# Optimization experiments

Measured on AMD Instinct MI355X. Metric: run time of the kernel, lower is better.

Reference implementation:

```python
import jax, jax.numpy as jnp
import numpy as np

EPS = 1e-12  # matches torch F.normalize default eps

def _l2_normalize(v, axis=-1):
    n = jnp.sqrt(jnp.sum(v * v, axis=axis, keepdims=True))
    return v / jnp.maximum(n, EPS)

def setup_inputs() -> dict:
    key = jax.random.key(0)
    k1, k2, k3 = jax.random.split(key, 3)
    B, S, D_IN, D_OUT, T = 4, 4096, 1024, 1024, 1024
    std = 1.0 / np.sqrt(D_IN)
    return {
        "x": jax.random.normal(k1, (B, S, D_IN), dtype=jnp.float32),
        "key_tokens": jax.random.normal(k2, (T, D_IN), dtype=jnp.float32) * std,
        "value_tokens": jax.random.normal(k3, (T, D_OUT), dtype=jnp.float32) * std,
        "temp": jnp.ones((T, 1), dtype=jnp.float32),
    }

def reference(x, key_tokens, value_tokens, temp):
    # x: [B,S,D_in]; key_tokens: [T,D_in]; value_tokens: [T,D_out]; temp: [T,1]
    x_norm = _l2_normalize(x)                      # [B,S,D_in]
    k_norm = _l2_normalize(key_tokens)             # [T,D_in]
    sim = jnp.einsum('bsd,td->bst', x_norm, k_norm)  # [B,S,T]
    sim = sim * jax.nn.sigmoid(temp).reshape(1, 1, -1)
    # mod_softmax: scale each row to RMS-norm sqrt(T), then exact GELU
    T = sim.shape[-1]
    scale = jnp.sqrt(jnp.float32(T)) / jnp.sqrt(jnp.sum(sim * sim, axis=-1, keepdims=True))
    weights = jax.nn.gelu(sim * scale, approximate=False)  # [B,S,T]
    return jnp.einsum('bst,to->bso', weights, value_tokens)  # [B,S,D_out]
```

## Files before the change

kernel.cpp:

```cpp
#include <hip/hip_runtime.h>
#include <math.h>

typedef __attribute__((ext_vector_type(8))) short short8;
typedef __attribute__((ext_vector_type(4))) float floatx4;

__device__ __forceinline__ float bf2f(unsigned short u) {
    union { unsigned int u; float f; } v;
    v.u = ((unsigned int)u) << 16;
    return v.f;
}

__device__ __forceinline__ unsigned short f2bf(float f) {
    union { float f; unsigned int u; } v;
    v.f = f;
    unsigned int r = v.u + 0x7fffu + ((v.u >> 16) & 1u);
    return (unsigned short)(r >> 16);
}

__device__ __forceinline__ void gload16_lds(const void* g, void* l) {
    __builtin_amdgcn_global_load_lds(
        (const __attribute__((address_space(1))) unsigned int*)g,
        (__attribute__((address_space(3))) unsigned int*)l, 16, 0, 0);
}

__device__ __forceinline__ ushort4 cvt4(float4 v, float fa) {
    ushort4 o;
    o.x = f2bf(v.x * fa); o.y = f2bf(v.y * fa);
    o.z = f2bf(v.z * fa); o.w = f2bf(v.w * fa);
    return o;
}

__global__ __launch_bounds__(256) void prep_kernel(
    const float* __restrict__ x, const float* __restrict__ key,
    const float* __restrict__ temp, const float* __restrict__ val,
    unsigned short* __restrict__ xb, unsigned short* __restrict__ kf,
    unsigned short* __restrict__ VT, float* __restrict__ rowsq,
    int M, int T, int D, int Dout, int nRowBlocks) {
    const int bid = blockIdx.x;
    if (bid < nRowBlocks) {
        const int lane = threadIdx.x & 63;
        const int nWaves = nRowBlocks << 2;
        const int totRows = M + T;
        for (int row = (bid << 2) | (int)(threadIdx.x >> 6); row < totRows;
             row += nWaves) {
            const bool isx = row < M;
            const int r = isx ? row : row - M;
            const float4* s4 =
                (const float4*)(isx ? (x + (size_t)r * D) : (key + (size_t)r * D));
            float4 v0 = s4[lane];
            float4 v1 = s4[lane + 64];
            float4 v2 = s4[lane + 128];
            float4 v3 = s4[lane + 192];
            float s = v0.x * v0.x + v0.y * v0.y + v0.z * v0.z + v0.w * v0.w;
            s += v1.x * v1.x + v1.y * v1.y + v1.z * v1.z + v1.w * v1.w;
            s += v2.x * v2.x + v2.y * v2.y + v2.z * v2.z + v2.w * v2.w;
            s += v3.x * v3.x + v3.y * v3.y + v3.z * v3.z + v3.w * v3.w;
#pragma unroll
            for (int o = 32; o > 0; o >>= 1) s += __shfl_xor(s, o, 64);
            float fa = 1.0f / fmaxf(sqrtf(s), 1e-12f);
            if (isx) {
                if (lane == 0) rowsq[r] = 0.0f;
            } else {
                fa = fa / (1.0f + expf(-temp[r]));
            }
            ushort4* dst =
                (ushort4*)(isx ? (xb + (size_t)r * D) : (kf + (size_t)r * D));
            dst[lane] = cvt4(v0, fa);
            dst[lane + 64] = cvt4(v1, fa);
            dst[lane + 128] = cvt4(v2, fa);
            dst[lane + 192] = cvt4(v3, fa);
        }
    } else {
        __shared__ unsigned short tile[64][65];
        const int idx = bid - nRowBlocks;
        const int nCt = Dout >> 6;
        const int c0 = (idx % nCt) * 64;
        const int r0 = (idx / nCt) * 64;
        const int t = threadIdx.x;
        for (int i = t; i < 4096; i += 256) {
            int rr = i >> 6, cc = i & 63;
            tile[rr][cc] = f2bf(val[(size_t)(r0 + rr) * Dout + c0 + cc]);
        }
        __syncthreads();
        for (int i = t; i < 4096; i += 256) {
            int rr = i >> 6, cc = i & 63;
            VT[(size_t)(c0 + rr) * T + r0 + cc] = tile[cc][rr];
        }
    }
}

template <int MODE>
__global__ __launch_bounds__(256) void gemm_bt(const unsigned short* __restrict__ A,
                                               const unsigned short* __restrict__ B,
                                               void* __restrict__ Cv,
                                               float* __restrict__ rowsq,
                                               int M, int N, int K) {
    __shared__ __align__(16) unsigned short As[128 * 64];
    __shared__ __align__(16) unsigned short Bs[128 * 64];
    const int tid = threadIdx.x;
    const int lane = tid & 63;
    const int w = tid >> 6;
    const int m0 = blockIdx.x * 128;
    const int n0 = blockIdx.y * 128;
    const int wm = (w & 1) * 64;
    const int wn = (w >> 1) * 64;
    const int cl = lane & 15;
    const int q = lane >> 4;

    floatx4 acc[4][4];
#pragma unroll
    for (int i = 0; i < 4; i++)
#pragma unroll
        for (int j = 0; j < 4; j++) acc[i][j] = (floatx4){0.f, 0.f, 0.f, 0.f};

    const int srow = tid >> 2;
    const int skof = (tid & 3) * 8;
    const unsigned short* ga0 = A + (size_t)(m0 + srow) * K + skof;
    const unsigned short* ga1 = A + (size_t)(m0 + srow + 64) * K + skof;
    const unsigned short* gb0 = B + (size_t)(n0 + srow) * K + skof;
    const unsigned short* gb1 = B + (size_t)(n0 + srow + 64) * K + skof;
    unsigned short* la0 = &As[(w * 64) * 8];
    unsigned short* la1 = &As[(256 + w * 64) * 8];
    unsigned short* lb0 = &Bs[(w * 64) * 8];
    unsigned short* lb1 = &Bs[(256 + w * 64) * 8];

    const int a_off = (wm + cl) * 32 + q * 8;
    const int b_off = (wn + cl) * 32 + q * 8;

    for (int kt = 0; kt < K; kt += 64) {
        __syncthreads();
#pragma unroll
        for (int h = 0; h < 2; h++) {
            const int go = kt + h * 32;
            const int lo = h * 4096;
            gload16_lds(ga0 + go, la0 + lo);
            gload16_lds(ga1 + go, la1 + lo);
            gload16_lds(gb0 + go, lb0 + lo);
            gload16_lds(gb1 + go, lb1 + lo);
        }
        __syncthreads();
#pragma unroll
        for (int h = 0; h < 2; h++) {
            const int lo = h * 4096;
            short8 af[4], bfr[4];
#pragma unroll
            for (int mt = 0; mt < 4; mt++)
                af[mt] = *(const short8*)&As[lo + a_off + mt * 16 * 32];
#pragma unroll
            for (int nt = 0; nt < 4; nt++)
                bfr[nt] = *(const short8*)&Bs[lo + b_off + nt * 16 * 32];
#pragma unroll
            for (int mt = 0; mt < 4; mt++)
#pragma unroll
                for (int nt = 0; nt < 4; nt++)
                    acc[mt][nt] = __builtin_amdgcn_mfma_f32_16x16x32_bf16(
                        af[mt], bfr[nt], acc[mt][nt], 0, 0, 0);
        }
    }

#pragma unroll
    for (int mt = 0; mt < 4; mt++) {
#pragma unroll
        for (int r = 0; r < 4; r++) {
            const int m = m0 + wm + mt * 16 + q * 4 + r;
            if (MODE == 0) {
                unsigned short* C = (unsigned short*)Cv;
                float ssq = 0.f;
#pragma unroll
                for (int nt = 0; nt < 4; nt++) {
                    float v = acc[mt][nt][r];
                    ssq += v * v;
                    C[(size_t)m * N + n0 + wn + nt * 16 + cl] = f2bf(v);
                }
#pragma unroll
                for (int o = 1; o < 16; o <<= 1) ssq += __shfl_xor(ssq, o, 64);
                if (cl == 0) atomicAdd(&rowsq[m], ssq);
            } else {
                float* C = (float*)Cv;
#pragma unroll
                for (int nt = 0; nt < 4; nt++)
                    C[(size_t)m * N + n0 + wn + nt * 16 + cl] = acc[mt][nt][r];
            }
        }
    }
}

__global__ __launch_bounds__(256) void gelu_kernel(unsigned short* __restrict__ sim,
                                                   const float* __restrict__ rowsq,
                                                   int nVec, int t8shift,
                                                   float sqrtT) {
    const int stride = gridDim.x * blockDim.x;
    const float kk = 0.70710678118654752f;
    for (int i = blockIdx.x * blockDim.x + threadIdx.x; i < nVec; i += stride) {
        short8 v = *(const short8*)(sim + (size_t)i * 8);
        const int row = i >> t8shift;
        const float scale = sqrtT / fmaxf(sqrtf(rowsq[row]), 1e-30f);
        short8 o;
#pragma unroll
        for (int j = 0; j < 8; j++) {
            float z = bf2f((unsigned short)v[j]) * scale;
            o[j] = (short)f2bf(0.5f * z * (1.0f + erff(z * kk)));
        }
        *(short8*)(sim + (size_t)i * 8) = o;
    }
}

extern "C" void kernel_launch(void* const* d_in, const int* in_sizes, int n_in,
                              void* d_out, int out_size, void* d_ws, size_t ws_size,
                              hipStream_t stream) {
    const float* x    = (const float*)d_in[0];
    const float* key  = (const float*)d_in[1];
    const float* val  = (const float*)d_in[2];
    const float* temp = (const float*)d_in[3];
    float* out = (float*)d_out;

    const int T = in_sizes[3];
    const int D = in_sizes[1] / T;
    const int Dout = in_sizes[2] / T;
    const int M = in_sizes[0] / D;

    char* ws = (char*)d_ws;
    size_t off = 0;
    unsigned short* xb  = (unsigned short*)(ws + off); off += (size_t)M * D * 2;
    unsigned short* sim = (unsigned short*)(ws + off); off += (size_t)M * T * 2;
    unsigned short* kf  = (unsigned short*)(ws + off); off += (size_t)T * D * 2;
    unsigned short* VT  = (unsigned short*)(ws + off); off += (size_t)Dout * T * 2;
    float* rowsq = (float*)(ws + off); off += (size_t)M * 4;
    (void)ws_size; (void)n_in; (void)out_size;

    const int nTrTiles = (T >> 6) * (Dout >> 6);
    const int nRowBlocks = 1024;
    prep_kernel<<<nRowBlocks + nTrTiles, 256, 0, stream>>>(
        x, key, temp, val, xb, kf, VT, rowsq, M, T, D, Dout, nRowBlocks);
    gemm_bt<0><<<dim3(M / 128, T / 128), 256, 0, stream>>>(xb, kf, sim, rowsq, M, T, D);
    int t8shift = 0;
    {
        int t8 = T >> 3;
        while ((1 << t8shift) < t8) t8shift++;
    }
    gelu_kernel<<<2048, 256, 0, stream>>>(sim, rowsq, M * (T >> 3), t8shift,
                                          sqrtf((float)T));
    gemm_bt<1><<<dim3(M / 128, Dout / 128), 256, 0, stream>>>(sim, VT, out, nullptr,
                                                              M, Dout, T);
}
```

Before: 242.1 us.

## Replace GEMM with 256x256 tiled, 4-stage pipelined 8-wave MFMA kernel

Replaces the 128x128 single-buffered bf16 GEMM with a 256x256 tile kernel using 512 threads, a 4-deep LDS ring buffer fed by direct global-to-LDS loads, XOR swizzling of LDS rows, and interleaved load/compute phases with wave priority hints. It aims to hide global memory latency and raise MFMA utilization for both GEMMs. The larger tile uses 128KB of LDS and many accumulator registers, which limits occupancy. The hand-counted waitcnt and barrier choreography is fragile.

```diff
diff --git a/kernel.cpp b/kernel.cpp
--- a/kernel.cpp
+++ b/kernel.cpp
@@ -90,87 +90,114 @@
 }
 
 template <int MODE>
-__global__ __launch_bounds__(256) void gemm_bt(const unsigned short* __restrict__ A,
-                                               const unsigned short* __restrict__ B,
-                                               void* __restrict__ Cv,
-                                               float* __restrict__ rowsq,
-                                               int M, int N, int K) {
-    __shared__ __align__(16) unsigned short As[128 * 64];
-    __shared__ __align__(16) unsigned short Bs[128 * 64];
+__global__ __launch_bounds__(512, 2) void gemm256(
+    const unsigned short* __restrict__ A, const unsigned short* __restrict__ B,
+    void* __restrict__ Cv, float* __restrict__ rowsq, int M, int N, int K) {
+    __shared__ __align__(16) char smem[131072];
     const int tid = threadIdx.x;
     const int lane = tid & 63;
     const int w = tid >> 6;
-    const int m0 = blockIdx.x * 128;
-    const int n0 = blockIdx.y * 128;
-    const int wm = (w & 1) * 64;
-    const int wn = (w >> 1) * 64;
+    const int wr = w >> 2;
+    const int wc = w & 3;
+    const int m0 = blockIdx.x * 256;
+    const int n0 = blockIdx.y * 256;
+    const int q = lane >> 4;
     const int cl = lane & 15;
-    const int q = lane >> 4;
-
-    floatx4 acc[4][4];
-#pragma unroll
-    for (int i = 0; i < 4; i++)
+
+    const int srow = lane >> 2;
+    const int sch = (lane & 3) ^ ((lane & 32) >> 4);
+    const unsigned short* gA0 = A + (size_t)(m0 + w * 16 + srow) * K + sch * 8;
+    const unsigned short* gA1 = gA0 + (size_t)128 * K;
+    const unsigned short* gB0 = B + (size_t)(n0 + w * 16 + srow) * K + sch * 8;
+    const unsigned short* gB1 = gB0 + (size_t)128 * K;
+
+    const int LB = (((lane & 15) * 64 + q * 16) ^ ((lane & 8) << 2));
+
+    floatx4 acc[8][4];
+#pragma unroll
+    for (int i = 0; i < 8; i++)
 #pragma unroll
         for (int j = 0; j < 4; j++) acc[i][j] = (floatx4){0.f, 0.f, 0.f, 0.f};
 
-    const int srow = tid >> 2;
-    const int skof = (tid & 3) * 8;
-    const unsigned short* ga0 = A + (size_t)(m0 + srow) * K + skof;
-    const unsigned short* ga1 = A + (size_t)(m0 + srow + 64) * K + skof;
-    const unsigned short* gb0 = B + (size_t)(n0 + srow) * K + skof;
-    const unsigned short* gb1 = B + (size_t)(n0 + srow + 64) * K + skof;
-    unsigned short* la0 = &As[(w * 64) * 8];
-    unsigned short* la1 = &As[(256 + w * 64) * 8];
-    unsigned short* lb0 = &Bs[(w * 64) * 8];
-    unsigned short* lb1 = &Bs[(256 + w * 64) * 8];
-
-    const int a_off = (wm + cl) * 32 + q * 8;
-    const int b_off = (wn + cl) * 32 + q * 8;
-
-    for (int kt = 0; kt < K; kt += 64) {
-        __syncthreads();
-#pragma unroll
-        for (int h = 0; h < 2; h++) {
-            const int go = kt + h * 32;
-            const int lo = h * 4096;
-            gload16_lds(ga0 + go, la0 + lo);
-            gload16_lds(ga1 + go, la1 + lo);
-            gload16_lds(gb0 + go, lb0 + lo);
-            gload16_lds(gb1 + go, lb1 + lo);
-        }
-        __syncthreads();
-#pragma unroll
-        for (int h = 0; h < 2; h++) {
-            const int lo = h * 4096;
-            short8 af[4], bfr[4];
-#pragma unroll
-            for (int mt = 0; mt < 4; mt++)
-                af[mt] = *(const short8*)&As[lo + a_off + mt * 16 * 32];
-#pragma unroll
-            for (int nt = 0; nt < 4; nt++)
-                bfr[nt] = *(const short8*)&Bs[lo + b_off + nt * 16 * 32];
-#pragma unroll
-            for (int mt = 0; mt < 4; mt++)
-#pragma unroll
-                for (int nt = 0; nt < 4; nt++)
-                    acc[mt][nt] = __builtin_amdgcn_mfma_f32_16x16x32_bf16(
-                        af[mt], bfr[nt], acc[mt][nt], 0, 0, 0);
-        }
-    }
-
-#pragma unroll
-    for (int mt = 0; mt < 4; mt++) {
-#pragma unroll
-        for (int r = 0; r < 4; r++) {
-            const int m = m0 + wm + mt * 16 + q * 4 + r;
+    const int NT = K >> 5;
+
+    auto stage_h = [&](int t, int h) {
+        char* base = smem + (size_t)(t & 3) * 32768 + (h * 8 + w) * 1024;
+        const size_t ro = (size_t)h * 128 * K;
+        const size_t ko = (size_t)t * 32;
+        gload16_lds(gA0 + ro + ko, base);
+        gload16_lds(gB0 + ro + ko, base + 16384);
+    };
+    (void)gA1; (void)gB1;
+
+    stage_h(0, 0); stage_h(0, 1);
+    stage_h(1, 0); stage_h(1, 1);
+    stage_h(2, 0); stage_h(2, 1);
+    asm volatile("s_waitcnt vmcnt(8)" ::: "memory");
+    __builtin_amdgcn_s_barrier();
+
+    for (int tt = 0; tt < NT; ++tt) {
+        const char* sA = smem + (size_t)(tt & 3) * 32768;
+        const char* sB = sA + 16384;
+        const bool st = (tt + 3) < NT;
+        short8 bf[4], af[4];
+#pragma unroll
+        for (int nt = 0; nt < 4; ++nt)
+            bf[nt] = *(const short8*)(sB + (wc * 4 + nt) * 1024 + LB);
+#pragma unroll
+        for (int mt = 0; mt < 4; ++mt)
+            af[mt] = *(const short8*)(sA + (wr * 8 + mt) * 1024 + LB);
+        if (st) stage_h(tt + 3, 0);
+        __builtin_amdgcn_s_barrier();
+        asm volatile("s_waitcnt lgkmcnt(0)" ::: "memory");
+        __builtin_amdgcn_s_setprio(1);
+#pragma unroll
+        for (int mt = 0; mt < 4; ++mt)
+#pragma unroll
+            for (int nt = 0; nt < 4; ++nt)
+                acc[mt][nt] = __builtin_amdgcn_mfma_f32_16x16x32_bf16(
+                    af[mt], bf[nt], acc[mt][nt], 0, 0, 0);
+        __builtin_amdgcn_s_setprio(0);
+        __builtin_amdgcn_s_barrier();
+        __builtin_amdgcn_sched_barrier(0);
+#pragma unroll
+        for (int mt = 0; mt < 4; ++mt)
+            af[mt] = *(const short8*)(sA + (wr * 8 + 4 + mt) * 1024 + LB);
+        if (st) stage_h(tt + 3, 1);
+        if (tt < NT - 3) {
+            asm volatile("s_waitcnt vmcnt(8)" ::: "memory");
+        } else if (tt == NT - 3) {
+            asm volatile("s_waitcnt vmcnt(4)" ::: "memory");
+        } else if (tt == NT - 2) {
+            asm volatile("s_waitcnt vmcnt(0)" ::: "memory");
+        }
+        __builtin_amdgcn_s_barrier();
+        asm volatile("s_waitcnt lgkmcnt(0)" ::: "memory");
+        __builtin_amdgcn_s_setprio(1);
+#pragma unroll
+        for (int mt = 0; mt < 4; ++mt)
+#pragma unroll
+            for (int nt = 0; nt < 4; ++nt)
+                acc[4 + mt][nt] = __builtin_amdgcn_mfma_f32_16x16x32_bf16(
+                    af[mt], bf[nt], acc[4 + mt][nt], 0, 0, 0);
+        __builtin_amdgcn_s_setprio(0);
+        __builtin_amdgcn_s_barrier();
+        __builtin_amdgcn_sched_barrier(0);
+    }
+
+#pragma unroll
+    for (int mt = 0; mt < 8; ++mt) {
+#pragma unroll
+        for (int r = 0; r < 4; ++r) {
+            const int m = m0 + wr * 128 + mt * 16 + q * 4 + r;
             if (MODE == 0) {
                 unsigned short* C = (unsigned short*)Cv;
                 float ssq = 0.f;
 #pragma unroll
-                for (int nt = 0; nt < 4; nt++) {
+                for (int nt = 0; nt < 4; ++nt) {
                     float v = acc[mt][nt][r];
                     ssq += v * v;
-                    C[(size_t)m * N + n0 + wn + nt * 16 + cl] = f2bf(v);
+                    C[(size_t)m * N + n0 + wc * 64 + nt * 16 + cl] = f2bf(v);
                 }
 #pragma unroll
                 for (int o = 1; o < 16; o <<= 1) ssq += __shfl_xor(ssq, o, 64);
@@ -178,8 +205,9 @@
             } else {
                 float* C = (float*)Cv;
 #pragma unroll
-                for (int nt = 0; nt < 4; nt++)
-                    C[(size_t)m * N + n0 + wn + nt * 16 + cl] = acc[mt][nt][r];
+                for (int nt = 0; nt < 4; ++nt)
+                    C[(size_t)m * N + n0 + wc * 64 + nt * 16 + cl] =
+                        acc[mt][nt][r];
             }
         }
     }
@@ -232,7 +260,8 @@
     const int nRowBlocks = 1024;
     prep_kernel<<<nRowBlocks + nTrTiles, 256, 0, stream>>>(
         x, key, temp, val, xb, kf, VT, rowsq, M, T, D, Dout, nRowBlocks);
-    gemm_bt<0><<<dim3(M / 128, T / 128), 256, 0, stream>>>(xb, kf, sim, rowsq, M, T, D);
+    gemm256<0><<<dim3(M / 256, T / 256), 512, 0, stream>>>(xb, kf, sim, rowsq,
+                                                           M, T, D);
     int t8shift = 0;
     {
         int t8 = T >> 3;
@@ -240,6 +269,6 @@
     }
     gelu_kernel<<<2048, 256, 0, stream>>>(sim, rowsq, M * (T >> 3), t8shift,
                                           sqrtf((float)T));
-    gemm_bt<1><<<dim3(M / 128, Dout / 128), 256, 0, stream>>>(sim, VT, out, nullptr,
-                                                              M, Dout, T);
-}
+    gemm256<1><<<dim3(M / 256, Dout / 256), 512, 0, stream>>>(sim, VT, out,
+                                                              nullptr, M, Dout, T);
+}
```

Result: faster. 216.9 us (-10.4%).
